# Kernel tuning notes

Measured on AMD Instinct MI355X. Metric: run time of the kernel, lower is better.

Reference implementation:

```python
import jax, jax.numpy as jnp
import numpy as np

EPS = 1e-06


def setup_inputs() -> dict:
    key = jax.random.key(0)
    k1, k2 = jax.random.split(key)
    B, T, E = 4, 4096, 1024
    M = E // 2
    x = jax.random.normal(k1, (B, T, E), dtype=jnp.float32)
    # causal mask: position i may attend to j <= i... note module multiplies K
    # (which is nonzero only for j >= i) by mask; a standard causal lower-tri
    # mask would zero everything but the diagonal. The module's bump kernel
    # looks FORWARD (diff = (j-i).clamp(min=0)), so the natural mask here is
    # upper-triangular (j >= i), i.e. the 'causal' mask for this pooling.
    mask = jnp.triu(jnp.ones((T, T), dtype=bool))
    gate_raw = jnp.full((M,), -3.0, dtype=jnp.float32)
    return {"x": x, "mask": mask, "gate_raw": gate_raw}


def reference(x, mask, gate_raw):
    B, T, E = x.shape
    dtype = x.dtype
    x_c = x[..., 0::2]                                  # (B, T, M) content channels

    # convex bump kernel K[i, j], nonzero for j >= i
    i = jnp.arange(T, dtype=dtype)[:, None]
    j = jnp.arange(T, dtype=dtype)[None, :]
    diff = jnp.maximum(j - i, 0.0)
    horizon = jnp.maximum(jnp.float32(T) - i, 1.0)
    u = jnp.minimum(diff / horizon, 1.0 - EPS)
    K = jnp.exp(1.0 - 1.0 / (1.0 - u * u + EPS))
    K = jnp.where(u >= 1.0 - EPS, jnp.asarray(EPS, dtype), K)

    K = K * mask.astype(dtype)
    K = K / jnp.maximum(K.sum(-1, keepdims=True), EPS)  # row-normalize

    phi = jnp.einsum('ij,bjm->bim', K, x_c)             # (B, T, M)
    gate = jax.nn.softplus(gate_raw)[None, None, :]     # (1, 1, M)
    out = x.at[..., 1::2].set(phi * gate)               # write phase channels
    return out
```

## Files before the change

### kernel.cpp

```cpp
#include <hip/hip_runtime.h>
#include <cstdint>
#include <cstddef>

#define Tdim 4096
#define Bdim 4
#define Edim 1024
#define Mdim 512
#define EPSF 1e-6f

typedef __bf16 bf16x8 __attribute__((ext_vector_type(8)));
typedef float f32x4 __attribute__((ext_vector_type(4)));

__device__ __forceinline__ unsigned short f2bf(float f) {
  union { float f; unsigned int u; } a; a.f = f;
  unsigned int r = a.u + 0x7fffu + ((a.u >> 16) & 1u);
  return (unsigned short)(r >> 16);
}

__device__ __forceinline__ unsigned int pack_bf16(float a, float b) {
  union { float f; unsigned int u; } ua, ub; ua.f = a; ub.f = b;
  return __builtin_amdgcn_perm(ub.u + 0x8000u, ua.u + 0x8000u, 0x07060302u);
}

__device__ __forceinline__ float kernel_g(float dj, float inv_h) {
  float u = fminf(dj * inv_h, 1.0f - EPSF);
  return __expf(1.0f - 1.0f / (1.0f - u * u + EPSF));
}

typedef void __attribute__((address_space(1)))* gas1;
typedef void __attribute__((address_space(3)))* las3;
__device__ __forceinline__ void load_lds16(const void* g, void* l) {
  __builtin_amdgcn_global_load_lds((gas1)(g), (las3)(l), 16, 0, 0);
}

__global__ __launch_bounds__(256) void prep_kernel(const float* __restrict__ x,
                                                   unsigned short* __restrict__ Kmat,
                                                   unsigned short* __restrict__ XcT) {
  __shared__ float smem[4104];
  const int tid = threadIdx.x;
  const int id = blockIdx.x;
  if (id < Tdim) {
    const int i = id;
    const float inv_h = __fdividef(1.0f, (float)(Tdim - i));
    float s = 0.0f;
    for (int j = i + tid; j < Tdim; j += 256) {
      const float g = kernel_g((float)(j - i), inv_h);
      smem[j] = g;
      s += g;
    }
#pragma unroll
    for (int off = 32; off; off >>= 1) s += __shfl_down(s, off);
    if ((tid & 63) == 0) smem[4096 + (tid >> 6)] = s;
    __syncthreads();
    const float inv_s = __fdividef(
        1.0f, fmaxf(smem[4096] + smem[4097] + smem[4098] + smem[4099], EPSF));
    unsigned short* row = Kmat + (size_t)i * Tdim;
#pragma unroll
    for (int q = tid; q < 512; q += 256) {
      const int j8 = q * 8;
      float v[8];
#pragma unroll
      for (int k = 0; k < 8; ++k) {
        const int j = j8 + k;
        v[k] = (j >= i) ? smem[j] * inv_s : 0.0f;
      }
      uint4 pk;
      pk.x = pack_bf16(v[0], v[1]);
      pk.y = pack_bf16(v[2], v[3]);
      pk.z = pack_bf16(v[4], v[5]);
      pk.w = pack_bf16(v[6], v[7]);
      *reinterpret_cast<uint4*>(&row[j8]) = pk;
    }
  } else {
    const int eid = id - Tdim;
    const int j0 = (eid & 63) * 64;
    const int m0 = ((eid >> 6) & 15) * 32;
    const int b  = eid >> 10;
    unsigned short* Ls = reinterpret_cast<unsigned short*>(smem);
    const int q = tid & 15;
    const int jbase = tid >> 4;
#pragma unroll
    for (int it = 0; it < 4; ++it) {
      const int jj = jbase + it * 16;
      const size_t off = ((size_t)(b * Tdim + j0 + jj)) * Edim + 2 * m0 + 4 * q;
      const float4 v = *reinterpret_cast<const float4*>(&x[off]);
      Ls[(2 * q) * 68 + jj]     = f2bf(v.x);
      Ls[(2 * q + 1) * 68 + jj] = f2bf(v.z);
    }
    __syncthreads();
    const int ch = tid & 15;
    const int mb = tid >> 4;
#pragma unroll
    for (int it = 0; it < 2; ++it) {
      const int m = mb + it * 16;
      ushort4 uv;
      uv.x = Ls[m * 68 + 4 * ch];
      uv.y = Ls[m * 68 + 4 * ch + 1];
      uv.z = Ls[m * 68 + 4 * ch + 2];
      uv.w = Ls[m * 68 + 4 * ch + 3];
      *reinterpret_cast<ushort4*>(
          &XcT[((size_t)(b * Mdim + m0 + m)) * Tdim + j0 + 4 * ch]) = uv;
    }
  }
}

__global__ __launch_bounds__(256) void gemm_kernel(
    const unsigned short* __restrict__ Kmat,
    const unsigned short* __restrict__ XcT,
    const float* __restrict__ x,
    const float* __restrict__ graw,
    float* __restrict__ out) {
  const int id = blockIdx.x;
  int p;
  if (id < 256) p = id >> 4;
  else          p = 31 - ((id - 256) >> 4);
  const int mb = id & 15;
  const int i0 = p * 128;
  const int m0 = (mb & 3) * 128;
  const int b  = mb >> 2;

  __shared__ unsigned short As[2][128 * 64];
  __shared__ unsigned short Bs[2][128 * 64];
  const int tid = threadIdx.x;
  const int w = tid >> 6;
  const int l = tid & 63;
  f32x4 acc[4][4] = {};
  const int wr = w >> 1, wc = w & 1;
  const unsigned short* Arow = Kmat + (size_t)i0 * Tdim;
  const unsigned short* Brow = XcT + ((size_t)b * Mdim + m0) * Tdim;
  const int srow  = l >> 3;
  const int sslot = l & 7;
  const int schunk = (sslot ^ srow) * 8;

#pragma unroll
  for (int t = 0; t < 4; ++t) {
    const int rr = (w * 4 + t) * 8 + srow;
    load_lds16(Arow + (size_t)rr * Tdim + (i0 + schunk), &As[0][(w * 4 + t) * 512]);
    load_lds16(Brow + (size_t)rr * Tdim + (i0 + schunk), &Bs[0][(w * 4 + t) * 512]);
  }

  int cur = 0;
  const int lr16 = l & 15;
  const int kq = l >> 4;
  for (int j0 = i0; j0 < Tdim; j0 += 64, cur ^= 1) {
    __syncthreads();
    const int jn = j0 + 64;
    if (jn < Tdim) {
#pragma unroll
      for (int t = 0; t < 4; ++t) {
        const int rr = (w * 4 + t) * 8 + srow;
        load_lds16(Arow + (size_t)rr * Tdim + (jn + schunk), &As[cur ^ 1][(w * 4 + t) * 512]);
        load_lds16(Brow + (size_t)rr * Tdim + (jn + schunk), &Bs[cur ^ 1][(w * 4 + t) * 512]);
      }
    }
#pragma unroll
    for (int kk = 0; kk < 2; ++kk) {
      bf16x8 af[4], bfr[4];
      const int chunk = kk * 4 + kq;
      const int slot = (chunk ^ (lr16 & 7)) * 8;
#pragma unroll
      for (int r = 0; r < 4; ++r)
        af[r] = *reinterpret_cast<const bf16x8*>(&As[cur][(wr * 64 + r * 16 + lr16) * 64 + slot]);
#pragma unroll
      for (int c = 0; c < 4; ++c)
        bfr[c] = *reinterpret_cast<const bf16x8*>(&Bs[cur][(wc * 64 + c * 16 + lr16) * 64 + slot]);
#pragma unroll
      for (int r = 0; r < 4; ++r)
#pragma unroll
        for (int c = 0; c < 4; ++c)
          acc[r][c] = __builtin_amdgcn_mfma_f32_16x16x32_bf16(af[r], bfr[c], acc[r][c], 0, 0, 0);
    }
  }

  const int lr = l & 15;
  const int lq = l >> 4;
  float gm[4];
#pragma unroll
  for (int c = 0; c < 4; ++c) {
    const float v = graw[m0 + wc * 64 + c * 16 + lr];
    gm[c] = fmaxf(v, 0.0f) + __logf(1.0f + __expf(-fabsf(v)));
  }
#pragma unroll
  for (int r = 0; r < 4; ++r) {
    const int ii = i0 + wr * 64 + r * 16 + lq * 4;
#pragma unroll
    for (int c = 0; c < 4; ++c) {
      const int m = m0 + wc * 64 + c * 16 + lr;
#pragma unroll
      for (int v = 0; v < 4; ++v) {
        const size_t o = ((size_t)(b * Tdim + ii + v)) * Edim + 2 * m;
        const float2 xv = *reinterpret_cast<const float2*>(&x[o]);
        float2 res;
        res.x = xv.x;
        res.y = acc[r][c][v] * gm[c];
        *reinterpret_cast<float2*>(&out[o]) = res;
      }
    }
  }
}

__global__ __launch_bounds__(256) void fallback_kernel(const float* __restrict__ x,
                                                       const float* __restrict__ graw,
                                                       float* __restrict__ out) {
  const int i = blockIdx.x, b = blockIdx.y, tid = threadIdx.x;
  const float inv_h = 1.0f / (float)(Tdim - i);
  float s = 0.0f;
  for (int j = i + tid; j < Tdim; j += 256)
    s += kernel_g((float)(j - i), inv_h);
#pragma unroll
  for (int off = 32; off; off >>= 1) s += __shfl_down(s, off);
  __shared__ float red[4];
  __shared__ float sinv_sh;
  if ((tid & 63) == 0) red[tid >> 6] = s;
  __syncthreads();
  if (tid == 0) sinv_sh = 1.0f / (red[0] + red[1] + red[2] + red[3]);
  __syncthreads();
  const float sinv = sinv_sh;
  const float* xb = x + (size_t)b * Tdim * Edim;
  float a0 = 0.0f, a1 = 0.0f;
  const int m0 = tid, m1 = tid + 256;
  for (int j = i; j < Tdim; ++j) {
    const float wgt = kernel_g((float)(j - i), inv_h);
    const float* xr = xb + (size_t)j * Edim;
    a0 += wgt * xr[2 * m0];
    a1 += wgt * xr[2 * m1];
  }
  const float v0 = graw[m0], v1 = graw[m1];
  const float g0 = fmaxf(v0, 0.0f) + log1pf(__expf(-fabsf(v0)));
  const float g1 = fmaxf(v1, 0.0f) + log1pf(__expf(-fabsf(v1)));
  const size_t o = ((size_t)(b * Tdim + i)) * Edim;
  const float* xi = xb + (size_t)i * Edim;
  out[o + 2 * m0]     = xi[2 * m0];
  out[o + 2 * m0 + 1] = a0 * sinv * g0;
  out[o + 2 * m1]     = xi[2 * m1];
  out[o + 2 * m1 + 1] = a1 * sinv * g1;
}

extern "C" void kernel_launch(void* const* d_in, const int* in_sizes, int n_in,
                              void* d_out, int out_size, void* d_ws, size_t ws_size,
                              hipStream_t stream) {
  const float* x = (const float*)d_in[0];
  const float* gate_raw = (const float*)d_in[2];
  float* out = (float*)d_out;

  const size_t XcT_bytes = (size_t)Bdim * Mdim * Tdim * 2;
  const size_t K_bytes   = (size_t)Tdim * Tdim * 2;
  const size_t need = XcT_bytes + K_bytes;

  if (ws_size < need) {
    fallback_kernel<<<dim3(Tdim, Bdim), 256, 0, stream>>>(x, gate_raw, out);
    return;
  }

  char* ws = (char*)d_ws;
  unsigned short* XcT  = (unsigned short*)ws;
  unsigned short* Kmat = (unsigned short*)(ws + XcT_bytes);

  prep_kernel<<<dim3(2 * Tdim), 256, 0, stream>>>(x, Kmat, XcT);
  gemm_kernel<<<dim3(512), 256, 0, stream>>>(Kmat, XcT, x, gate_raw, out);
}
```

Measured before the change: 227.6 us.

## Use persistent atomic work queue with smaller 64-row tiles in triangular GEMM

The GEMM becomes a persistent kernel. Blocks pull tiles from a global atomic counter, which prep_kernel resets, and tiles are issued longest-first (lowest i0 first) to balance the triangular workload. Row tiles shrink from 128 to 64, giving 1024 finer tiles with a 64x128 per-block output split across 4 waves. Prep also skips writing the all-zero lower part of each K row, since the GEMM never reads it. Smaller tiles reduce the MFMA work per load, and the atomic queue adds a small per-tile sync cost.

```diff
diff --git a/kernel.cpp b/kernel.cpp
--- a/kernel.cpp
+++ b/kernel.cpp
@@ -35,10 +35,12 @@
 
 __global__ __launch_bounds__(256) void prep_kernel(const float* __restrict__ x,
                                                    unsigned short* __restrict__ Kmat,
-                                                   unsigned short* __restrict__ XcT) {
+                                                   unsigned short* __restrict__ XcT,
+                                                   int* __restrict__ cnt) {
   __shared__ float smem[4104];
   const int tid = threadIdx.x;
   const int id = blockIdx.x;
+  if (id == 0 && tid == 0) *cnt = 0;
   if (id < Tdim) {
     const int i = id;
     const float inv_h = __fdividef(1.0f, (float)(Tdim - i));
@@ -55,8 +57,8 @@
     const float inv_s = __fdividef(
         1.0f, fmaxf(smem[4096] + smem[4097] + smem[4098] + smem[4099], EPSF));
     unsigned short* row = Kmat + (size_t)i * Tdim;
-#pragma unroll
-    for (int q = tid; q < 512; q += 256) {
+    const int q0 = (i >> 6) << 3;
+    for (int q = q0 + tid; q < 512; q += 256) {
       const int j8 = q * 8;
       float v[8];
 #pragma unroll
@@ -109,91 +111,103 @@
     const unsigned short* __restrict__ XcT,
     const float* __restrict__ x,
     const float* __restrict__ graw,
-    float* __restrict__ out) {
-  const int id = blockIdx.x;
-  int p;
-  if (id < 256) p = id >> 4;
-  else          p = 31 - ((id - 256) >> 4);
-  const int mb = id & 15;
-  const int i0 = p * 128;
-  const int m0 = (mb & 3) * 128;
-  const int b  = mb >> 2;
-
-  __shared__ unsigned short As[2][128 * 64];
+    float* __restrict__ out,
+    int* __restrict__ cnt) {
+  __shared__ unsigned short As[2][64 * 64];
   __shared__ unsigned short Bs[2][128 * 64];
+  __shared__ int s_q;
   const int tid = threadIdx.x;
   const int w = tid >> 6;
   const int l = tid & 63;
-  f32x4 acc[4][4] = {};
-  const int wr = w >> 1, wc = w & 1;
-  const unsigned short* Arow = Kmat + (size_t)i0 * Tdim;
-  const unsigned short* Brow = XcT + ((size_t)b * Mdim + m0) * Tdim;
   const int srow  = l >> 3;
   const int sslot = l & 7;
   const int schunk = (sslot ^ srow) * 8;
-
-#pragma unroll
-  for (int t = 0; t < 4; ++t) {
-    const int rr = (w * 4 + t) * 8 + srow;
-    load_lds16(Arow + (size_t)rr * Tdim + (i0 + schunk), &As[0][(w * 4 + t) * 512]);
-    load_lds16(Brow + (size_t)rr * Tdim + (i0 + schunk), &Bs[0][(w * 4 + t) * 512]);
-  }
-
-  int cur = 0;
   const int lr16 = l & 15;
   const int kq = l >> 4;
-  for (int j0 = i0; j0 < Tdim; j0 += 64, cur ^= 1) {
+
+  for (;;) {
+    if (tid == 0) s_q = atomicAdd(cnt, 1);
     __syncthreads();
-    const int jn = j0 + 64;
-    if (jn < Tdim) {
-#pragma unroll
-      for (int t = 0; t < 4; ++t) {
-        const int rr = (w * 4 + t) * 8 + srow;
-        load_lds16(Arow + (size_t)rr * Tdim + (jn + schunk), &As[cur ^ 1][(w * 4 + t) * 512]);
-        load_lds16(Brow + (size_t)rr * Tdim + (jn + schunk), &Bs[cur ^ 1][(w * 4 + t) * 512]);
-      }
-    }
-#pragma unroll
-    for (int kk = 0; kk < 2; ++kk) {
-      bf16x8 af[4], bfr[4];
-      const int chunk = kk * 4 + kq;
-      const int slot = (chunk ^ (lr16 & 7)) * 8;
-#pragma unroll
-      for (int r = 0; r < 4; ++r)
-        af[r] = *reinterpret_cast<const bf16x8*>(&As[cur][(wr * 64 + r * 16 + lr16) * 64 + slot]);
-#pragma unroll
-      for (int c = 0; c < 4; ++c)
-        bfr[c] = *reinterpret_cast<const bf16x8*>(&Bs[cur][(wc * 64 + c * 16 + lr16) * 64 + slot]);
-#pragma unroll
-      for (int r = 0; r < 4; ++r)
-#pragma unroll
-        for (int c = 0; c < 4; ++c)
-          acc[r][c] = __builtin_amdgcn_mfma_f32_16x16x32_bf16(af[r], bfr[c], acc[r][c], 0, 0, 0);
-    }
-  }
-
-  const int lr = l & 15;
-  const int lq = l >> 4;
-  float gm[4];
-#pragma unroll
-  for (int c = 0; c < 4; ++c) {
-    const float v = graw[m0 + wc * 64 + c * 16 + lr];
-    gm[c] = fmaxf(v, 0.0f) + __logf(1.0f + __expf(-fabsf(v)));
-  }
-#pragma unroll
-  for (int r = 0; r < 4; ++r) {
-    const int ii = i0 + wr * 64 + r * 16 + lq * 4;
-#pragma unroll
-    for (int c = 0; c < 4; ++c) {
-      const int m = m0 + wc * 64 + c * 16 + lr;
-#pragma unroll
-      for (int v = 0; v < 4; ++v) {
-        const size_t o = ((size_t)(b * Tdim + ii + v)) * Edim + 2 * m;
-        const float2 xv = *reinterpret_cast<const float2*>(&x[o]);
-        float2 res;
-        res.x = xv.x;
-        res.y = acc[r][c][v] * gm[c];
-        *reinterpret_cast<float2*>(&out[o]) = res;
+    const int q = s_q;
+    if (q >= 64 * 16) break;
+    const int p  = q >> 4;
+    const int mb = q & 15;
+    const int i0 = p * 64;
+    const int m0 = (mb & 3) * 128;
+    const int b  = mb >> 2;
+    const unsigned short* Arow = Kmat + (size_t)i0 * Tdim;
+    const unsigned short* Brow = XcT + ((size_t)b * Mdim + m0) * Tdim;
+    f32x4 acc[4][2] = {};
+
+#pragma unroll
+    for (int t = 0; t < 2; ++t) {
+      const int rr = (w * 2 + t) * 8 + srow;
+      load_lds16(Arow + (size_t)rr * Tdim + (i0 + schunk), &As[0][(w * 2 + t) * 512]);
+    }
+#pragma unroll
+    for (int t = 0; t < 4; ++t) {
+      const int rr = (w * 4 + t) * 8 + srow;
+      load_lds16(Brow + (size_t)rr * Tdim + (i0 + schunk), &Bs[0][(w * 4 + t) * 512]);
+    }
+
+    int cur = 0;
+    for (int j0 = i0; j0 < Tdim; j0 += 64, cur ^= 1) {
+      __syncthreads();
+      const int jn = j0 + 64;
+      if (jn < Tdim) {
+#pragma unroll
+        for (int t = 0; t < 2; ++t) {
+          const int rr = (w * 2 + t) * 8 + srow;
+          load_lds16(Arow + (size_t)rr * Tdim + (jn + schunk), &As[cur ^ 1][(w * 2 + t) * 512]);
+        }
+#pragma unroll
+        for (int t = 0; t < 4; ++t) {
+          const int rr = (w * 4 + t) * 8 + srow;
+          load_lds16(Brow + (size_t)rr * Tdim + (jn + schunk), &Bs[cur ^ 1][(w * 4 + t) * 512]);
+        }
+      }
+#pragma unroll
+      for (int kk = 0; kk < 2; ++kk) {
+        bf16x8 af[4], bfr[2];
+        const int chunk = kk * 4 + kq;
+        const int slot = (chunk ^ (lr16 & 7)) * 8;
+#pragma unroll
+        for (int r = 0; r < 4; ++r)
+          af[r] = *reinterpret_cast<const bf16x8*>(&As[cur][(r * 16 + lr16) * 64 + slot]);
+#pragma unroll
+        for (int c = 0; c < 2; ++c)
+          bfr[c] = *reinterpret_cast<const bf16x8*>(&Bs[cur][(w * 32 + c * 16 + lr16) * 64 + slot]);
+#pragma unroll
+        for (int r = 0; r < 4; ++r)
+#pragma unroll
+          for (int c = 0; c < 2; ++c)
+            acc[r][c] = __builtin_amdgcn_mfma_f32_16x16x32_bf16(af[r], bfr[c], acc[r][c], 0, 0, 0);
+      }
+    }
+
+    const int lr = l & 15;
+    const int lq = l >> 4;
+    float gm[2];
+#pragma unroll
+    for (int c = 0; c < 2; ++c) {
+      const float v = graw[m0 + w * 32 + c * 16 + lr];
+      gm[c] = fmaxf(v, 0.0f) + __logf(1.0f + __expf(-fabsf(v)));
+    }
+#pragma unroll
+    for (int r = 0; r < 4; ++r) {
+      const int ii = i0 + r * 16 + lq * 4;
+#pragma unroll
+      for (int c = 0; c < 2; ++c) {
+        const int m = m0 + w * 32 + c * 16 + lr;
+#pragma unroll
+        for (int v = 0; v < 4; ++v) {
+          const size_t o = ((size_t)(b * Tdim + ii + v)) * Edim + 2 * m;
+          const float2 xv = *reinterpret_cast<const float2*>(&x[o]);
+          float2 res;
+          res.x = xv.x;
+          res.y = acc[r][c][v] * gm[c];
+          *reinterpret_cast<float2*>(&out[o]) = res;
+        }
       }
     }
   }
@@ -245,7 +259,7 @@
 
   const size_t XcT_bytes = (size_t)Bdim * Mdim * Tdim * 2;
   const size_t K_bytes   = (size_t)Tdim * Tdim * 2;
-  const size_t need = XcT_bytes + K_bytes;
+  const size_t need = XcT_bytes + K_bytes + 16;
 
   if (ws_size < need) {
     fallback_kernel<<<dim3(Tdim, Bdim), 256, 0, stream>>>(x, gate_raw, out);
@@ -255,7 +269,8 @@
   char* ws = (char*)d_ws;
   unsigned short* XcT  = (unsigned short*)ws;
   unsigned short* Kmat = (unsigned short*)(ws + XcT_bytes);
-
-  prep_kernel<<<dim3(2 * Tdim), 256, 0, stream>>>(x, Kmat, XcT);
-  gemm_kernel<<<dim3(512), 256, 0, stream>>>(Kmat, XcT, x, gate_raw, out);
-}
+  int* cnt = (int*)(ws + XcT_bytes + K_bytes);
+
+  prep_kernel<<<dim3(2 * Tdim), 256, 0, stream>>>(x, Kmat, XcT, cnt);
+  gemm_kernel<<<dim3(768), 256, 0, stream>>>(Kmat, XcT, x, gate_raw, out, cnt);
+}
```

Result: slower. 238.8 us (+4.9%).

## Deepen GEMM LDS pipeline to four stages with k-major layout

Applied to the files above, without the earlier changes.

Replaces the double-buffered 64-wide K tile with a four-buffer, 32-wide ring. Loads are issued two stages ahead and waited on with explicit vmcnt and a raw s_barrier instead of __syncthreads. The LDS layout becomes k-chunk-major, with rows contiguous per 8-element chunk, so the XOR swizzle is dropped. The K-matrix prep now writes only from each row's 128-aligned block onward, skipping the all-zero lower-triangle stores the GEMM never reads; this adds more barriers per unit of work and a risk of bank conflicts.

```diff
diff --git a/kernel.cpp b/kernel.cpp
--- a/kernel.cpp
+++ b/kernel.cpp
@@ -55,8 +55,8 @@
     const float inv_s = __fdividef(
         1.0f, fmaxf(smem[4096] + smem[4097] + smem[4098] + smem[4099], EPSF));
     unsigned short* row = Kmat + (size_t)i * Tdim;
-#pragma unroll
-    for (int q = tid; q < 512; q += 256) {
+    const int q0 = (i >> 7) << 4;
+    for (int q = q0 + tid; q < 512; q += 256) {
       const int j8 = q * 8;
       float v[8];
 #pragma unroll
@@ -110,6 +110,8 @@
     const float* __restrict__ x,
     const float* __restrict__ graw,
     float* __restrict__ out) {
+  __shared__ unsigned short As[4][128 * 32];
+  __shared__ unsigned short Bs[4][128 * 32];
   const int id = blockIdx.x;
   int p;
   if (id < 256) p = id >> 4;
@@ -118,59 +120,57 @@
   const int i0 = p * 128;
   const int m0 = (mb & 3) * 128;
   const int b  = mb >> 2;
-
-  __shared__ unsigned short As[2][128 * 64];
-  __shared__ unsigned short Bs[2][128 * 64];
   const int tid = threadIdx.x;
   const int w = tid >> 6;
   const int l = tid & 63;
-  f32x4 acc[4][4] = {};
   const int wr = w >> 1, wc = w & 1;
   const unsigned short* Arow = Kmat + (size_t)i0 * Tdim;
   const unsigned short* Brow = XcT + ((size_t)b * Mdim + m0) * Tdim;
-  const int srow  = l >> 3;
-  const int sslot = l & 7;
-  const int schunk = (sslot ^ srow) * 8;
-
-#pragma unroll
-  for (int t = 0; t < 4; ++t) {
-    const int rr = (w * 4 + t) * 8 + srow;
-    load_lds16(Arow + (size_t)rr * Tdim + (i0 + schunk), &As[0][(w * 4 + t) * 512]);
-    load_lds16(Brow + (size_t)rr * Tdim + (i0 + schunk), &Bs[0][(w * 4 + t) * 512]);
-  }
-
-  int cur = 0;
+
+  const int g0 = (2 * w) * 64 + l;
+  const int g1 = g0 + 64;
+  const size_t aoff0 = (size_t)(g0 & 127) * Tdim + (g0 >> 7) * 8;
+  const size_t aoff1 = (size_t)(g1 & 127) * Tdim + (g1 >> 7) * 8;
+  f32x4 acc[4][4] = {};
+
+#define STAGE(bufi, jt)                                                     \
+  do {                                                                      \
+    load_lds16(Arow + aoff0 + (jt), &As[(bufi)][(2 * w) * 512]);            \
+    load_lds16(Arow + aoff1 + (jt), &As[(bufi)][(2 * w + 1) * 512]);        \
+    load_lds16(Brow + aoff0 + (jt), &Bs[(bufi)][(2 * w) * 512]);            \
+    load_lds16(Brow + aoff1 + (jt), &Bs[(bufi)][(2 * w + 1) * 512]);        \
+  } while (0)
+
+  const int n = (Tdim - i0) >> 5;
+  STAGE(0, i0);
+  STAGE(1, i0 + 32);
+
   const int lr16 = l & 15;
   const int kq = l >> 4;
-  for (int j0 = i0; j0 < Tdim; j0 += 64, cur ^= 1) {
-    __syncthreads();
-    const int jn = j0 + 64;
-    if (jn < Tdim) {
-#pragma unroll
-      for (int t = 0; t < 4; ++t) {
-        const int rr = (w * 4 + t) * 8 + srow;
-        load_lds16(Arow + (size_t)rr * Tdim + (jn + schunk), &As[cur ^ 1][(w * 4 + t) * 512]);
-        load_lds16(Brow + (size_t)rr * Tdim + (jn + schunk), &Bs[cur ^ 1][(w * 4 + t) * 512]);
-      }
-    }
-#pragma unroll
-    for (int kk = 0; kk < 2; ++kk) {
-      bf16x8 af[4], bfr[4];
-      const int chunk = kk * 4 + kq;
-      const int slot = (chunk ^ (lr16 & 7)) * 8;
-#pragma unroll
-      for (int r = 0; r < 4; ++r)
-        af[r] = *reinterpret_cast<const bf16x8*>(&As[cur][(wr * 64 + r * 16 + lr16) * 64 + slot]);
+  int jt = i0;
+  for (int t = 0; t < n; ++t, jt += 32) {
+    const int jc = (jt + 64 <= Tdim - 32) ? (jt + 64) : (Tdim - 32);
+    STAGE((t + 2) & 3, jc);
+    asm volatile("s_waitcnt vmcnt(8)" ::: "memory");
+    __builtin_amdgcn_s_barrier();
+    __builtin_amdgcn_sched_barrier(0);
+    const int buf = t & 3;
+    bf16x8 af[4], bfr[4];
+#pragma unroll
+    for (int r = 0; r < 4; ++r)
+      af[r] = *reinterpret_cast<const bf16x8*>(
+          &As[buf][(kq * 128 + wr * 64 + r * 16 + lr16) * 8]);
+#pragma unroll
+    for (int c = 0; c < 4; ++c)
+      bfr[c] = *reinterpret_cast<const bf16x8*>(
+          &Bs[buf][(kq * 128 + wc * 64 + c * 16 + lr16) * 8]);
+#pragma unroll
+    for (int r = 0; r < 4; ++r)
 #pragma unroll
       for (int c = 0; c < 4; ++c)
-        bfr[c] = *reinterpret_cast<const bf16x8*>(&Bs[cur][(wc * 64 + c * 16 + lr16) * 64 + slot]);
-#pragma unroll
-      for (int r = 0; r < 4; ++r)
-#pragma unroll
-        for (int c = 0; c < 4; ++c)
-          acc[r][c] = __builtin_amdgcn_mfma_f32_16x16x32_bf16(af[r], bfr[c], acc[r][c], 0, 0, 0);
-    }
-  }
+        acc[r][c] = __builtin_amdgcn_mfma_f32_16x16x32_bf16(af[r], bfr[c], acc[r][c], 0, 0, 0);
+  }
+#undef STAGE
 
   const int lr = l & 15;
   const int lq = l >> 4;
```

Result: slower. 253.2 us (+11.3%).

## Prepack K into MFMA-fragment tiles and load A operand directly to registers

Applied to the files above, without the earlier changes.

The dense 4096x4096 bf16 K matrix is replaced by a packed set of only the upper-triangular 128x64 tiles, stored in the register-fragment order the MFMA expects. A new packK kernel builds these tiles from per-row inverse sums, which prep_kernel now writes. The GEMM then reads A fragments straight from global memory into registers, skipping the LDS staging. This cuts the K write and read traffic and frees half the LDS. The cost is an extra kernel launch and global-latency-bound A loads inside the main loop.

```diff
diff --git a/kernel.cpp b/kernel.cpp
--- a/kernel.cpp
+++ b/kernel.cpp
@@ -7,9 +7,12 @@
 #define Edim 1024
 #define Mdim 512
 #define EPSF 1e-6f
+#define NTILES 1056
 
 typedef __bf16 bf16x8 __attribute__((ext_vector_type(8)));
 typedef float f32x4 __attribute__((ext_vector_type(4)));
+
+__host__ __device__ __forceinline__ int panel_start(int p) { return p * (65 - p); }
 
 __device__ __forceinline__ unsigned short f2bf(float f) {
   union { float f; unsigned int u; } a; a.f = f;
@@ -34,43 +37,24 @@
 }
 
 __global__ __launch_bounds__(256) void prep_kernel(const float* __restrict__ x,
-                                                   unsigned short* __restrict__ Kmat,
+                                                   float* __restrict__ inv_s,
                                                    unsigned short* __restrict__ XcT) {
-  __shared__ float smem[4104];
+  __shared__ float smem[1104];
   const int tid = threadIdx.x;
   const int id = blockIdx.x;
   if (id < Tdim) {
     const int i = id;
     const float inv_h = __fdividef(1.0f, (float)(Tdim - i));
     float s = 0.0f;
-    for (int j = i + tid; j < Tdim; j += 256) {
-      const float g = kernel_g((float)(j - i), inv_h);
-      smem[j] = g;
-      s += g;
-    }
+    for (int j = i + tid; j < Tdim; j += 256)
+      s += kernel_g((float)(j - i), inv_h);
 #pragma unroll
     for (int off = 32; off; off >>= 1) s += __shfl_down(s, off);
-    if ((tid & 63) == 0) smem[4096 + (tid >> 6)] = s;
+    if ((tid & 63) == 0) smem[1088 + (tid >> 6)] = s;
     __syncthreads();
-    const float inv_s = __fdividef(
-        1.0f, fmaxf(smem[4096] + smem[4097] + smem[4098] + smem[4099], EPSF));
-    unsigned short* row = Kmat + (size_t)i * Tdim;
-#pragma unroll
-    for (int q = tid; q < 512; q += 256) {
-      const int j8 = q * 8;
-      float v[8];
-#pragma unroll
-      for (int k = 0; k < 8; ++k) {
-        const int j = j8 + k;
-        v[k] = (j >= i) ? smem[j] * inv_s : 0.0f;
-      }
-      uint4 pk;
-      pk.x = pack_bf16(v[0], v[1]);
-      pk.y = pack_bf16(v[2], v[3]);
-      pk.z = pack_bf16(v[4], v[5]);
-      pk.w = pack_bf16(v[6], v[7]);
-      *reinterpret_cast<uint4*>(&row[j8]) = pk;
-    }
+    if (tid == 0)
+      inv_s[i] = __fdividef(
+          1.0f, fmaxf(smem[1088] + smem[1089] + smem[1090] + smem[1091], EPSF));
   } else {
     const int eid = id - Tdim;
     const int j0 = (eid & 63) * 64;
@@ -104,12 +88,50 @@
   }
 }
 
+__global__ __launch_bounds__(256) void packK_kernel(const float* __restrict__ inv_s,
+                                                    unsigned short* __restrict__ Kswz) {
+  const int id = blockIdx.x;
+  int p = 0;
+  while (id >= (p + 1) * (64 - p)) ++p;
+  const int jt = id - panel_start(p);
+  const int i0 = p * 128;
+  const int jb0 = i0 + jt * 64;
+  unsigned short* dst = Kswz + (size_t)id * 8192;
+  const int tid = threadIdx.x;
+#pragma unroll
+  for (int ss = 0; ss < 4; ++ss) {
+    const int G = ss * 256 + tid;
+    const int lane = G & 63;
+    const int kk = (G >> 6) & 1;
+    const int r  = (G >> 7) & 3;
+    const int h  = G >> 9;
+    const int li = h * 64 + r * 16 + (lane & 15);
+    const int i  = i0 + li;
+    const float inv_h = __fdividef(1.0f, (float)(Tdim - i));
+    const float sinv = inv_s[i];
+    const int jb = jb0 + (kk * 4 + (lane >> 4)) * 8;
+    float v[8];
+#pragma unroll
+    for (int e = 0; e < 8; ++e) {
+      const int j = jb + e;
+      v[e] = (j >= i) ? kernel_g((float)(j - i), inv_h) * sinv : 0.0f;
+    }
+    uint4 pk;
+    pk.x = pack_bf16(v[0], v[1]);
+    pk.y = pack_bf16(v[2], v[3]);
+    pk.z = pack_bf16(v[4], v[5]);
+    pk.w = pack_bf16(v[6], v[7]);
+    *reinterpret_cast<uint4*>(&dst[(size_t)G * 8]) = pk;
+  }
+}
+
 __global__ __launch_bounds__(256) void gemm_kernel(
-    const unsigned short* __restrict__ Kmat,
+    const unsigned short* __restrict__ Kswz,
     const unsigned short* __restrict__ XcT,
     const float* __restrict__ x,
     const float* __restrict__ graw,
     float* __restrict__ out) {
+  __shared__ unsigned short Bs[2][128 * 64];
   const int id = blockIdx.x;
   int p;
   if (id < 256) p = id >> 4;
@@ -118,57 +140,60 @@
   const int i0 = p * 128;
   const int m0 = (mb & 3) * 128;
   const int b  = mb >> 2;
-
-  __shared__ unsigned short As[2][128 * 64];
-  __shared__ unsigned short Bs[2][128 * 64];
   const int tid = threadIdx.x;
   const int w = tid >> 6;
   const int l = tid & 63;
-  f32x4 acc[4][4] = {};
   const int wr = w >> 1, wc = w & 1;
-  const unsigned short* Arow = Kmat + (size_t)i0 * Tdim;
   const unsigned short* Brow = XcT + ((size_t)b * Mdim + m0) * Tdim;
   const int srow  = l >> 3;
   const int sslot = l & 7;
   const int schunk = (sslot ^ srow) * 8;
+  const unsigned short* Apan =
+      Kswz + (size_t)panel_start(p) * 8192 + (size_t)(wr * 8) * 512 + (size_t)l * 8;
+
+  f32x4 acc[4][4] = {};
+  const int n = (Tdim - i0) >> 6;
 
 #pragma unroll
   for (int t = 0; t < 4; ++t) {
     const int rr = (w * 4 + t) * 8 + srow;
-    load_lds16(Arow + (size_t)rr * Tdim + (i0 + schunk), &As[0][(w * 4 + t) * 512]);
     load_lds16(Brow + (size_t)rr * Tdim + (i0 + schunk), &Bs[0][(w * 4 + t) * 512]);
   }
 
-  int cur = 0;
   const int lr16 = l & 15;
   const int kq = l >> 4;
-  for (int j0 = i0; j0 < Tdim; j0 += 64, cur ^= 1) {
+  int cur = 0;
+  for (int t = 0; t < n; ++t, cur ^= 1) {
     __syncthreads();
-    const int jn = j0 + 64;
-    if (jn < Tdim) {
-#pragma unroll
-      for (int t = 0; t < 4; ++t) {
-        const int rr = (w * 4 + t) * 8 + srow;
-        load_lds16(Arow + (size_t)rr * Tdim + (jn + schunk), &As[cur ^ 1][(w * 4 + t) * 512]);
-        load_lds16(Brow + (size_t)rr * Tdim + (jn + schunk), &Bs[cur ^ 1][(w * 4 + t) * 512]);
+    const unsigned short* At = Apan + (size_t)t * 8192;
+    bf16x8 af[2][4];
+#pragma unroll
+    for (int r = 0; r < 4; ++r) {
+      af[0][r] = *reinterpret_cast<const bf16x8*>(At + (r * 2 + 0) * 512);
+      af[1][r] = *reinterpret_cast<const bf16x8*>(At + (r * 2 + 1) * 512);
+    }
+    __builtin_amdgcn_sched_barrier(0);
+    if (t + 1 < n) {
+      const int jn = i0 + (t + 1) * 64;
+#pragma unroll
+      for (int q = 0; q < 4; ++q) {
+        const int rr = (w * 4 + q) * 8 + srow;
+        load_lds16(Brow + (size_t)rr * Tdim + (jn + schunk), &Bs[cur ^ 1][(w * 4 + q) * 512]);
       }
     }
 #pragma unroll
     for (int kk = 0; kk < 2; ++kk) {
-      bf16x8 af[4], bfr[4];
+      bf16x8 bfr[4];
       const int chunk = kk * 4 + kq;
       const int slot = (chunk ^ (lr16 & 7)) * 8;
 #pragma unroll
-      for (int r = 0; r < 4; ++r)
-        af[r] = *reinterpret_cast<const bf16x8*>(&As[cur][(wr * 64 + r * 16 + lr16) * 64 + slot]);
-#pragma unroll
       for (int c = 0; c < 4; ++c)
         bfr[c] = *reinterpret_cast<const bf16x8*>(&Bs[cur][(wc * 64 + c * 16 + lr16) * 64 + slot]);
 #pragma unroll
       for (int r = 0; r < 4; ++r)
 #pragma unroll
         for (int c = 0; c < 4; ++c)
-          acc[r][c] = __builtin_amdgcn_mfma_f32_16x16x32_bf16(af[r], bfr[c], acc[r][c], 0, 0, 0);
+          acc[r][c] = __builtin_amdgcn_mfma_f32_16x16x32_bf16(af[kk][r], bfr[c], acc[r][c], 0, 0, 0);
     }
   }
 
@@ -243,9 +268,10 @@
   const float* gate_raw = (const float*)d_in[2];
   float* out = (float*)d_out;
 
-  const size_t XcT_bytes = (size_t)Bdim * Mdim * Tdim * 2;
-  const size_t K_bytes   = (size_t)Tdim * Tdim * 2;
-  const size_t need = XcT_bytes + K_bytes;
+  const size_t XcT_bytes  = (size_t)Bdim * Mdim * Tdim * 2;
+  const size_t Kswz_bytes = (size_t)NTILES * 16384;
+  const size_t inv_bytes  = (size_t)Tdim * 4;
+  const size_t need = XcT_bytes + Kswz_bytes + inv_bytes;
 
   if (ws_size < need) {
     fallback_kernel<<<dim3(Tdim, Bdim), 256, 0, stream>>>(x, gate_raw, out);
@@ -254,8 +280,10 @@
 
   char* ws = (char*)d_ws;
   unsigned short* XcT  = (unsigned short*)ws;
-  unsigned short* Kmat = (unsigned short*)(ws + XcT_bytes);
-
-  prep_kernel<<<dim3(2 * Tdim), 256, 0, stream>>>(x, Kmat, XcT);
-  gemm_kernel<<<dim3(512), 256, 0, stream>>>(Kmat, XcT, x, gate_raw, out);
-}
+  unsigned short* Kswz = (unsigned short*)(ws + XcT_bytes);
+  float* inv_s         = (float*)(ws + XcT_bytes + Kswz_bytes);
+
+  prep_kernel<<<dim3(2 * Tdim), 256, 0, stream>>>(x, inv_s, XcT);
+  packK_kernel<<<dim3(NTILES), 256, 0, stream>>>(inv_s, Kswz);
+  gemm_kernel<<<dim3(512), 256, 0, stream>>>(Kswz, XcT, x, gate_raw, out);
+}
```

New measurement: 227.5 us. No clear change (-0.0%).
